# Optimization experiments

Hardware: AMD Instinct MI355X
Metric: run time of the kernel (lower is better)

Reference implementation:

```python
import jax, jax.numpy as jnp
import numpy as np

D_MODEL = 1024
NUM_HEAD = 16
D_HEAD = D_MODEL // NUM_HEAD


def setup_inputs() -> dict:
    key = jax.random.key(0)
    kx, kq, kk, kv, ko = jax.random.split(key, 5)
    x = jax.random.normal(kx, (2, 2048, D_MODEL), dtype=jnp.float32)
    p_q = jax.random.normal(kq, (D_MODEL, D_MODEL), dtype=jnp.float32)
    p_k = jax.random.normal(kk, (D_MODEL, D_MODEL), dtype=jnp.float32)
    p_v = jax.random.normal(kv, (D_MODEL, D_MODEL), dtype=jnp.float32)
    p_o = jax.random.normal(ko, (D_MODEL, D_MODEL), dtype=jnp.float32)
    return {"x": x, "p_q": p_q, "p_k": p_k, "p_v": p_v, "p_o": p_o}


def reference(x, p_q, p_k, p_v, p_o):
    B, S, _ = x.shape
    # project: weight viewed as [H, d_head, d_model]; out[b,h,s,d] = sum_m x[b,s,m] W[h,d,m]
    wq = p_q.reshape(NUM_HEAD, D_HEAD, D_MODEL)
    wk = p_k.reshape(NUM_HEAD, D_HEAD, D_MODEL)
    wv = p_v.reshape(NUM_HEAD, D_HEAD, D_MODEL)
    q = jnp.einsum('bsm,hdm->bhsd', x, wq)
    k = jnp.einsum('bsm,hdm->bhsd', x, wk)
    v = jnp.einsum('bsm,hdm->bhsd', x, wv)
    # full causal attention, scores scaled by 1/sqrt(d_head)
    scores = jnp.einsum('bhqd,bhkd->bhqk', q, k) / jnp.sqrt(jnp.float32(D_HEAD))
    causal = jnp.tril(jnp.ones((S, S), dtype=bool))
    scores = jnp.where(causal, scores, -jnp.inf)
    attn = jax.nn.softmax(scores, axis=-1)
    out = jnp.einsum('bhqk,bhkd->bhqd', attn, v)
    out = out.transpose(0, 2, 1, 3).reshape(B, S, D_MODEL)  # [B,S,H*d_head]
    # output proj: einsum '... d1, d2 d1 -> ... d2' == out @ p_o.T
    return jnp.einsum('bsm,nm->bsn', out, p_o)
```

## Files before the change

### kernel.cpp

```cpp
#include <hip/hip_runtime.h>
#include <stdint.h>

#define D_MODEL 1024
#define SEQ     2048
#define NHEAD   16
#define BATCH   2
#define NROWS   (BATCH*SEQ)

typedef _Float16 f16;
typedef _Float16 f16x8 __attribute__((ext_vector_type(8)));
typedef _Float16 f16x4 __attribute__((ext_vector_type(4)));
typedef __fp16   h16x2 __attribute__((ext_vector_type(2)));
typedef float    f32x4 __attribute__((ext_vector_type(4)));

#define MFMA16 __builtin_amdgcn_mfma_f32_16x16x32_f16

__device__ __forceinline__ void gload16(const void* g, void* l) {
  __builtin_amdgcn_global_load_lds(
      (const __attribute__((address_space(1))) void*)g,
      (__attribute__((address_space(3))) void*)l, 16, 0, 0);
}

__device__ __forceinline__ int pkh2(float a, float b) {
  union { h16x2 h; int i; } u;
  u.h = __builtin_amdgcn_cvt_pkrtz(a, b);
  return u.i;
}

__global__ void split4_kernel(const float* __restrict__ in, f16* __restrict__ hi,
                              f16* __restrict__ lo, int n4, float scale) {
  int i = blockIdx.x * blockDim.x + threadIdx.x;
  if (i >= n4) return;
  float4 v = reinterpret_cast<const float4*>(in)[i];
  v.x *= scale; v.y *= scale; v.z *= scale; v.w *= scale;
  f16x4 h, l4;
  h[0] = (f16)v.x; h[1] = (f16)v.y; h[2] = (f16)v.z; h[3] = (f16)v.w;
  l4[0] = (f16)(v.x - (float)h[0]);
  l4[1] = (f16)(v.y - (float)h[1]);
  l4[2] = (f16)(v.z - (float)h[2]);
  l4[3] = (f16)(v.w - (float)h[3]);
  *reinterpret_cast<f16x4*>(hi + 4*(size_t)i) = h;
  *reinterpret_cast<f16x4*>(lo + 4*(size_t)i) = l4;
}

__global__ void prep_w_kernel(const float* __restrict__ pq, const float* __restrict__ pk,
                              const float* __restrict__ pv, const float* __restrict__ po,
                              f16* __restrict__ wq_hi, f16* __restrict__ wq_lo,
                              f16* __restrict__ wk_hi, f16* __restrict__ wk_lo,
                              f16* __restrict__ wv_h,  f16* __restrict__ wo_h,
                              int n4, float qscale) {
  int i = blockIdx.x * blockDim.x + threadIdx.x;
  if (i >= n4) return;
  {
    float4 v = reinterpret_cast<const float4*>(pq)[i];
    v.x *= qscale; v.y *= qscale; v.z *= qscale; v.w *= qscale;
    f16x4 h, l4;
    h[0] = (f16)v.x; h[1] = (f16)v.y; h[2] = (f16)v.z; h[3] = (f16)v.w;
    l4[0] = (f16)(v.x - (float)h[0]); l4[1] = (f16)(v.y - (float)h[1]);
    l4[2] = (f16)(v.z - (float)h[2]); l4[3] = (f16)(v.w - (float)h[3]);
    *reinterpret_cast<f16x4*>(wq_hi + 4*(size_t)i) = h;
    *reinterpret_cast<f16x4*>(wq_lo + 4*(size_t)i) = l4;
  }
  {
    float4 v = reinterpret_cast<const float4*>(pk)[i];
    f16x4 h, l4;
    h[0] = (f16)v.x; h[1] = (f16)v.y; h[2] = (f16)v.z; h[3] = (f16)v.w;
    l4[0] = (f16)(v.x - (float)h[0]); l4[1] = (f16)(v.y - (float)h[1]);
    l4[2] = (f16)(v.z - (float)h[2]); l4[3] = (f16)(v.w - (float)h[3]);
    *reinterpret_cast<f16x4*>(wk_hi + 4*(size_t)i) = h;
    *reinterpret_cast<f16x4*>(wk_lo + 4*(size_t)i) = l4;
  }
  {
    float4 v = reinterpret_cast<const float4*>(pv)[i];
    f16x4 h;
    h[0] = (f16)v.x; h[1] = (f16)v.y; h[2] = (f16)v.z; h[3] = (f16)v.w;
    *reinterpret_cast<f16x4*>(wv_h + 4*(size_t)i) = h;
  }
  {
    float4 v = reinterpret_cast<const float4*>(po)[i];
    f16x4 h;
    h[0] = (f16)v.x; h[1] = (f16)v.y; h[2] = (f16)v.z; h[3] = (f16)v.w;
    *reinterpret_cast<f16x4*>(wo_h + 4*(size_t)i) = h;
  }
}

template<bool SPLIT_IN, bool SPLIT_OUT, bool F32_OUT, bool COLCHUNK>
__global__ __launch_bounds__(256, 2)
void gemm_nt(const f16* __restrict__ Ahi, const f16* __restrict__ Alo,
             const f16* __restrict__ Bhi, const f16* __restrict__ Blo,
             f16* __restrict__ Chi, f16* __restrict__ Clo, float* __restrict__ Cf,
             int M, int N, int K)
{
  constexpr int ALO_OFF = 8192;
  constexpr int B_OFF   = SPLIT_IN ? 16384 : 8192;
  constexpr int BLO_OFF = 20480;
  constexpr int STRIDE  = SPLIT_IN ? 24576 : 12288;
  __shared__ __align__(16) char smem[2 * STRIDE];

  const int tid = threadIdx.x;
  const int w = tid >> 6, l = tid & 63;
  const int wr = (w >> 1) * 64;
  const int wc = (w & 1) * 32;

  const int gx = gridDim.x, gy = gridDim.y;
  const int nwg = gx * gy;
  const int flat = blockIdx.y * gx + blockIdx.x;
  const int swz = (flat & 7) * (nwg >> 3) + (flat >> 3);
  const int bxn = COLCHUNK ? (swz / gy) : (swz % gx);
  const int byn = COLCHUNK ? (swz % gy) : (swz / gx);
  const int bm = byn * 128, bn = bxn * 64;

  f32x4 acc[4][2] = {};

  const int srow = tid >> 2;
  const int schunk = 8 * (((tid & 3) ^ ((srow >> 1) & 3)));

  auto stage = [&](int kt) {
    char* dst = smem + (kt & 1) * STRIDE;
    const int k0 = kt * 32;
    const f16* ga = Ahi + (size_t)(bm + srow) * K + k0 + schunk;
    gload16(ga,        dst + (w << 10));
    gload16(ga + 64*K, dst + 4096 + (w << 10));
    const f16* gb = Bhi + (size_t)(bn + srow) * K + k0 + schunk;
    gload16(gb,        dst + B_OFF + (w << 10));
    if (SPLIT_IN) {
      const f16* gal = Alo + (size_t)(bm + srow) * K + k0 + schunk;
      gload16(gal,        dst + ALO_OFF + (w << 10));
      gload16(gal + 64*K, dst + ALO_OFF + 4096 + (w << 10));
      const f16* gbl = Blo + (size_t)(bn + srow) * K + k0 + schunk;
      gload16(gbl,        dst + BLO_OFF + (w << 10));
    }
  };

  const int nkt = K >> 5;
  stage(0);

  for (int kt = 0; kt < nkt; kt++) {
    if (kt + 1 < nkt) {
      stage(kt + 1);
      if constexpr (SPLIT_IN) asm volatile("s_waitcnt vmcnt(6)" ::: "memory");
      else                    asm volatile("s_waitcnt vmcnt(3)" ::: "memory");
    } else {
      asm volatile("s_waitcnt vmcnt(0)" ::: "memory");
    }
    __builtin_amdgcn_s_barrier();

    const char* buf = smem + (kt & 1) * STRIDE;
    const int ar = (l & 15);
    const int ak = 16 * ((l >> 4) ^ ((ar >> 1) & 3));
    f16x8 a_hi[4], a_lo[4];
#pragma unroll
    for (int mi = 0; mi < 4; mi++) {
      a_hi[mi] = *(const f16x8*)(buf + (size_t)(wr + mi*16 + ar) * 64 + ak);
      if (SPLIT_IN)
        a_lo[mi] = *(const f16x8*)(buf + ALO_OFF + (size_t)(wr + mi*16 + ar) * 64 + ak);
    }
    __builtin_amdgcn_s_setprio(1);
#pragma unroll
    for (int ni = 0; ni < 2; ni++) {
      f16x8 b_hi = *(const f16x8*)(buf + B_OFF + (size_t)(wc + ni*16 + ar) * 64 + ak);
      f16x8 b_lo = {};
      if (SPLIT_IN)
        b_lo = *(const f16x8*)(buf + BLO_OFF + (size_t)(wc + ni*16 + ar) * 64 + ak);
#pragma unroll
      for (int mi = 0; mi < 4; mi++) {
        acc[mi][ni] = MFMA16(a_hi[mi], b_hi, acc[mi][ni], 0, 0, 0);
        if (SPLIT_IN) {
          acc[mi][ni] = MFMA16(a_hi[mi], b_lo, acc[mi][ni], 0, 0, 0);
          acc[mi][ni] = MFMA16(a_lo[mi], b_hi, acc[mi][ni], 0, 0, 0);
        }
      }
    }
    __builtin_amdgcn_s_setprio(0);
    __builtin_amdgcn_s_barrier();
  }

  const int crow0 = bm + wr + (l >> 4) * 4;
  const int ccol0 = bn + wc + (l & 15);
#pragma unroll
  for (int mi = 0; mi < 4; mi++) {
#pragma unroll
    for (int ni = 0; ni < 2; ni++) {
#pragma unroll
      for (int j = 0; j < 4; j++) {
        size_t idx = (size_t)(crow0 + mi*16 + j) * N + (ccol0 + ni*16);
        float v = acc[mi][ni][j];
        if (F32_OUT) {
          Cf[idx] = v;
        } else {
          f16 h = (f16)v;
          Chi[idx] = h;
          if (SPLIT_OUT) Clo[idx] = (f16)(v - (float)h);
        }
      }
    }
  }
}

__global__ __launch_bounds__(512, 4)
void attn_kernel(const f16* __restrict__ Qhi, const f16* __restrict__ Qlo,
                 const f16* __restrict__ Khi, const f16* __restrict__ Klo,
                 const f16* __restrict__ VT, f16* __restrict__ Out)
{
  __shared__ __align__(16) char smem[49152];

  const int tid = threadIdx.x, w = tid >> 6, l = tid & 63;
  const int g = l >> 4, q4 = l & 15;
  const int flat = blockIdx.x;
  const int xcd = flat & 7, slot = flat >> 3;
  const int r4 = slot >> 4;
  const int ii = slot & 15;
  const int bh = xcd * 4 + r4;
  const int qx = ((slot >> 5) & 1) ? (15 - ii) : ii;
  const int b = bh >> 4, h = bh & 15;
  const int q0 = qx * 128;
  const int qw = q0 + w * 16;
  const int bS = b * SEQ;
  const size_t hoff = (size_t)h * 64;
  const int niter = 2 * qx + 2;

  f16x8 qh[2], ql[2];
#pragma unroll
  for (int ks = 0; ks < 2; ks++) {
    const size_t base = (size_t)(bS + qw + q4) * D_MODEL + hoff + ks * 32 + g * 8;
    qh[ks] = *(const f16x8*)(Qhi + base);
    ql[ks] = *(const f16x8*)(Qlo + base);
  }

  f32x4 o[4] = {};
  float m_run = -INFINITY, l_run = 0.f;

  const int src_off = 8 * ((l & 7) ^ (l >> 3));
  const int rowloc = w * 8 + (l >> 3);

  auto stage = [&](int t) {
    char* dst = smem + (t & 1) * 24576;
    const int kv0 = t * 64;
    const size_t krow = (size_t)(bS + kv0 + rowloc) * D_MODEL + hoff + src_off;
    gload16(Khi + krow, dst + (w << 10));
    gload16(Klo + krow, dst + 8192 + (w << 10));
    const size_t vrow = (hoff + rowloc) * (size_t)NROWS + bS + kv0 + src_off;
    gload16(VT + vrow, dst + 16384 + (w << 10));
  };

  const int idx_lo = (q4 + 32 * (g & 1)) * 4;
  const int idx_hi = idx_lo + 64;
  const bool upper = (l >= 32);

  stage(0);

  for (int t = 0; t < niter; t++) {
    if (t + 1 < niter) {
      stage(t + 1);
      asm volatile("s_waitcnt vmcnt(3)" ::: "memory");
    } else {
      asm volatile("s_waitcnt vmcnt(0)" ::: "memory");
    }
    __builtin_amdgcn_s_barrier();

    const int kv0 = t * 64;
    if (kv0 <= qw + 15) {
      const char* buf = smem + (t & 1) * 24576;

      f32x4 s[4] = {};
      __builtin_amdgcn_s_setprio(1);
#pragma unroll
      for (int ni = 0; ni < 4; ni++) {
        const int row = ni * 16 + q4;
#pragma unroll
        for (int ks = 0; ks < 2; ks++) {
          const int boff = row * 128 + 16 * ((ks * 4 + g) ^ (row & 7));
          f16x8 kh8 = *(const f16x8*)(buf + boff);
          f16x8 kl8 = *(const f16x8*)(buf + 8192 + boff);
          s[ni] = MFMA16(kh8, qh[ks], s[ni], 0, 0, 0);
          s[ni] = MFMA16(kh8, ql[ks], s[ni], 0, 0, 0);
          s[ni] = MFMA16(kl8, qh[ks], s[ni], 0, 0, 0);
        }
      }
      __builtin_amdgcn_s_setprio(0);

      const bool need_mask = (kv0 + 63) > qw;
      const int q_abs = qw + q4;
      float p[4][4];
      float pm = -INFINITY;
#pragma unroll
      for (int ni = 0; ni < 4; ni++)
#pragma unroll
        for (int j = 0; j < 4; j++) {
          float v = s[ni][j];
          if (need_mask && (kv0 + ni*16 + 4*g + j) > q_abs) v = -INFINITY;
          p[ni][j] = v;
          pm = fmaxf(pm, v);
        }
      pm = fmaxf(pm, __shfl_xor(pm, 16));
      pm = fmaxf(pm, __shfl_xor(pm, 32));

      const float mn = fmaxf(m_run, pm);
      const float sc = __builtin_amdgcn_exp2f(m_run - mn);
      m_run = mn;
      float ps = 0.f;
#pragma unroll
      for (int ni = 0; ni < 4; ni++)
#pragma unroll
        for (int j = 0; j < 4; j++) {
          const float e = __builtin_amdgcn_exp2f(p[ni][j] - mn);
          p[ni][j] = e;
          ps += e;
        }
      ps += __shfl_xor(ps, 16);
      ps += __shfl_xor(ps, 32);
      l_run = l_run * sc + ps;
#pragma unroll
      for (int nd = 0; nd < 4; nd++)
#pragma unroll
        for (int j = 0; j < 4; j++) o[nd][j] *= sc;

      f16x8 pa[2];
#pragma unroll
      for (int h2 = 0; h2 < 2; h2++) {
        const int pk0 = pkh2(p[2*h2][0],   p[2*h2][1]);
        const int pk1 = pkh2(p[2*h2][2],   p[2*h2][3]);
        const int pk2 = pkh2(p[2*h2+1][0], p[2*h2+1][1]);
        const int pk3 = pkh2(p[2*h2+1][2], p[2*h2+1][3]);
        const int b0l = __builtin_amdgcn_ds_bpermute(idx_lo, pk0);
        const int b2l = __builtin_amdgcn_ds_bpermute(idx_lo, pk2);
        const int b1l = __builtin_amdgcn_ds_bpermute(idx_lo, pk1);
        const int b3l = __builtin_amdgcn_ds_bpermute(idx_lo, pk3);
        const int b0h = __builtin_amdgcn_ds_bpermute(idx_hi, pk0);
        const int b2h = __builtin_amdgcn_ds_bpermute(idx_hi, pk2);
        const int b1h = __builtin_amdgcn_ds_bpermute(idx_hi, pk1);
        const int b3h = __builtin_amdgcn_ds_bpermute(idx_hi, pk3);
        union { int u[4]; f16x8 v; } pu;
        pu.u[0] = upper ? b2l : b0l;
        pu.u[1] = upper ? b3l : b1l;
        pu.u[2] = upper ? b2h : b0h;
        pu.u[3] = upper ? b3h : b1h;
        pa[h2] = pu.v;
      }

      __builtin_amdgcn_s_setprio(1);
#pragma unroll
      for (int nd = 0; nd < 4; nd++) {
        const int d = nd * 16 + q4;
#pragma unroll
        for (int h2 = 0; h2 < 2; h2++) {
          f16x8 bv = *(const f16x8*)(buf + 16384 + d * 128 + 16 * ((h2 * 4 + g) ^ (d & 7)));
          o[nd] = MFMA16(bv, pa[h2], o[nd], 0, 0, 0);
        }
      }
      __builtin_amdgcn_s_setprio(0);
    }
    __builtin_amdgcn_s_barrier();
  }

  const float inv = 1.0f / l_run;
  const size_t rowb = (size_t)(bS + qw + q4) * D_MODEL + hoff;
#pragma unroll
  for (int nd = 0; nd < 4; nd++) {
    f16x4 v;
#pragma unroll
    for (int j = 0; j < 4; j++) v[j] = (f16)(o[nd][j] * inv);
    *reinterpret_cast<f16x4*>(Out + rowb + nd * 16 + 4 * g) = v;
  }
}

extern "C" void kernel_launch(void* const* d_in, const int* in_sizes, int n_in,
                              void* d_out, int out_size, void* d_ws, size_t ws_size,
                              hipStream_t stream) {
  const float* x  = (const float*)d_in[0];
  const float* pq = (const float*)d_in[1];
  const float* pk = (const float*)d_in[2];
  const float* pv = (const float*)d_in[3];
  const float* po = (const float*)d_in[4];
  float* out = (float*)d_out;

  char* ws = (char*)d_ws;
  size_t off = 0;
  auto alloc = [&](size_t elems) {
    f16* p = (f16*)(ws + off);
    off += ((elems * 2 + 255) & ~(size_t)255);
    return p;
  };
  f16* x_hi  = alloc((size_t)NROWS * D_MODEL);
  f16* x_lo  = alloc((size_t)NROWS * D_MODEL);
  f16* wq_hi = alloc((size_t)D_MODEL * D_MODEL);
  f16* wq_lo = alloc((size_t)D_MODEL * D_MODEL);
  f16* wk_hi = alloc((size_t)D_MODEL * D_MODEL);
  f16* wk_lo = alloc((size_t)D_MODEL * D_MODEL);
  f16* wv_h  = alloc((size_t)D_MODEL * D_MODEL);
  f16* wo_h  = alloc((size_t)D_MODEL * D_MODEL);
  f16* q_hi  = alloc((size_t)NROWS * D_MODEL);
  f16* q_lo  = alloc((size_t)NROWS * D_MODEL);
  f16* k_hi  = alloc((size_t)NROWS * D_MODEL);
  f16* k_lo  = alloc((size_t)NROWS * D_MODEL);
  f16* vt    = alloc((size_t)NROWS * D_MODEL);
  f16* ao    = alloc((size_t)NROWS * D_MODEL);

  const int n4x = NROWS * D_MODEL / 4;
  const int n4w = D_MODEL * D_MODEL / 4;
  const float qscale = 0.125f * 1.44269504088896f;
  split4_kernel<<<n4x/256, 256, 0, stream>>>(x, x_hi, x_lo, n4x, 1.0f);
  prep_w_kernel<<<n4w/256, 256, 0, stream>>>(pq, pk, pv, po,
                                             wq_hi, wq_lo, wk_hi, wk_lo, wv_h, wo_h,
                                             n4w, qscale);

  dim3 gg(D_MODEL/64, NROWS/128);
  gemm_nt<true,  true,  false, false><<<gg, 256, 0, stream>>>(x_hi, x_lo, wq_hi, wq_lo, q_hi, q_lo, nullptr, NROWS, D_MODEL, D_MODEL);
  gemm_nt<true,  true,  false, false><<<gg, 256, 0, stream>>>(x_hi, x_lo, wk_hi, wk_lo, k_hi, k_lo, nullptr, NROWS, D_MODEL, D_MODEL);
  dim3 gv(NROWS/64, D_MODEL/128);
  gemm_nt<false, false, false, true><<<gv, 256, 0, stream>>>(wv_h, nullptr, x_hi, nullptr, vt, nullptr, nullptr, D_MODEL, NROWS, D_MODEL);

  attn_kernel<<<dim3(512), 512, 0, stream>>>(q_hi, q_lo, k_hi, k_lo, vt, ao);

  gemm_nt<false, false, true, false><<<gg, 256, 0, stream>>>(ao, nullptr, wo_h, nullptr, nullptr, nullptr, out, NROWS, D_MODEL, D_MODEL);
}
```

Measured before the change: 178.5 us.

## Software-pipeline QK^T one tile ahead and skip rescale when max grows little

Restructures the attention loop so K tiles are double-buffered and V tiles triple-buffered, with loads issued two tiles ahead and the QK^T MFMAs for tile t+1 computed before the softmax/PV of tile t. It also adds a lazy rescale: the running max and output rescale are updated only when some lane's new max exceeds the old one by more than 8 (in log2 units). The aim is to overlap memory latency and MFMA work with softmax and to cut per-iteration rescale ALU work. In exchange it uses more LDS (56KB), which may lower occupancy, adds an extra barrier per iteration, and lets probabilities exceed 1 by up to 2^8 before being converted to fp16.

```diff
diff --git a/kernel.cpp b/kernel.cpp
--- a/kernel.cpp
+++ b/kernel.cpp
@@ -202,7 +202,7 @@
                  const f16* __restrict__ Khi, const f16* __restrict__ Klo,
                  const f16* __restrict__ VT, f16* __restrict__ Out)
 {
-  __shared__ __align__(16) char smem[49152];
+  __shared__ __align__(16) char smem[57344];
 
   const int tid = threadIdx.x, w = tid >> 6, l = tid & 63;
   const int g = l >> 4, q4 = l & 15;
@@ -234,13 +234,36 @@
   const int rowloc = w * 8 + (l >> 3);
 
   auto stage = [&](int t) {
-    char* dst = smem + (t & 1) * 24576;
     const int kv0 = t * 64;
+    char* kdst = smem + (t & 1) * 16384 + (w << 10);
     const size_t krow = (size_t)(bS + kv0 + rowloc) * D_MODEL + hoff + src_off;
-    gload16(Khi + krow, dst + (w << 10));
-    gload16(Klo + krow, dst + 8192 + (w << 10));
+    gload16(Khi + krow, kdst);
+    gload16(Klo + krow, kdst + 8192);
+    char* vdst = smem + 32768 + (t % 3) * 8192 + (w << 10);
     const size_t vrow = (hoff + rowloc) * (size_t)NROWS + bS + kv0 + src_off;
-    gload16(VT + vrow, dst + 16384 + (w << 10));
+    gload16(VT + vrow, vdst);
+  };
+
+  f32x4 scur[4] = {};
+  auto qkt = [&](int t) {
+    const char* kb = smem + (t & 1) * 16384;
+    __builtin_amdgcn_s_setprio(1);
+#pragma unroll
+    for (int ni = 0; ni < 4; ni++) {
+      const int row = ni * 16 + q4;
+      f32x4 acc = {};
+#pragma unroll
+      for (int ks = 0; ks < 2; ks++) {
+        const int boff = row * 128 + 16 * ((ks * 4 + g) ^ (row & 7));
+        f16x8 kh8 = *(const f16x8*)(kb + boff);
+        f16x8 kl8 = *(const f16x8*)(kb + 8192 + boff);
+        acc = MFMA16(kh8, qh[ks], acc, 0, 0, 0);
+        acc = MFMA16(kh8, ql[ks], acc, 0, 0, 0);
+        acc = MFMA16(kl8, qh[ks], acc, 0, 0, 0);
+      }
+      scur[ni] = acc;
+    }
+    __builtin_amdgcn_s_setprio(0);
   };
 
   const int idx_lo = (q4 + 32 * (g & 1)) * 4;
@@ -248,37 +271,19 @@
   const bool upper = (l >= 32);
 
   stage(0);
+  stage(1);
+  asm volatile("s_waitcnt vmcnt(3)" ::: "memory");
+  __builtin_amdgcn_s_barrier();
+  qkt(0);
+  __builtin_amdgcn_s_barrier();
 
   for (int t = 0; t < niter; t++) {
-    if (t + 1 < niter) {
-      stage(t + 1);
-      asm volatile("s_waitcnt vmcnt(3)" ::: "memory");
-    } else {
-      asm volatile("s_waitcnt vmcnt(0)" ::: "memory");
-    }
-    __builtin_amdgcn_s_barrier();
+    const bool hasn = (t + 1 < niter);
+    const bool st2  = (t + 2 < niter);
+    if (st2) stage(t + 2);
 
     const int kv0 = t * 64;
     if (kv0 <= qw + 15) {
-      const char* buf = smem + (t & 1) * 24576;
-
-      f32x4 s[4] = {};
-      __builtin_amdgcn_s_setprio(1);
-#pragma unroll
-      for (int ni = 0; ni < 4; ni++) {
-        const int row = ni * 16 + q4;
-#pragma unroll
-        for (int ks = 0; ks < 2; ks++) {
-          const int boff = row * 128 + 16 * ((ks * 4 + g) ^ (row & 7));
-          f16x8 kh8 = *(const f16x8*)(buf + boff);
-          f16x8 kl8 = *(const f16x8*)(buf + 8192 + boff);
-          s[ni] = MFMA16(kh8, qh[ks], s[ni], 0, 0, 0);
-          s[ni] = MFMA16(kh8, ql[ks], s[ni], 0, 0, 0);
-          s[ni] = MFMA16(kl8, qh[ks], s[ni], 0, 0, 0);
-        }
-      }
-      __builtin_amdgcn_s_setprio(0);
-
       const bool need_mask = (kv0 + 63) > qw;
       const int q_abs = qw + q4;
       float p[4][4];
@@ -287,7 +292,7 @@
       for (int ni = 0; ni < 4; ni++)
 #pragma unroll
         for (int j = 0; j < 4; j++) {
-          float v = s[ni][j];
+          float v = scur[ni][j];
           if (need_mask && (kv0 + ni*16 + 4*g + j) > q_abs) v = -INFINITY;
           p[ni][j] = v;
           pm = fmaxf(pm, v);
@@ -295,25 +300,28 @@
       pm = fmaxf(pm, __shfl_xor(pm, 16));
       pm = fmaxf(pm, __shfl_xor(pm, 32));
 
-      const float mn = fmaxf(m_run, pm);
-      const float sc = __builtin_amdgcn_exp2f(m_run - mn);
-      m_run = mn;
+      if (!__all(pm - m_run <= 8.0f)) {
+        const float mn = fmaxf(m_run, pm);
+        const float sc = __builtin_amdgcn_exp2f(m_run - mn);
+        m_run = mn;
+        l_run *= sc;
+#pragma unroll
+        for (int nd = 0; nd < 4; nd++)
+#pragma unroll
+          for (int j = 0; j < 4; j++) o[nd][j] *= sc;
+      }
       float ps = 0.f;
 #pragma unroll
       for (int ni = 0; ni < 4; ni++)
 #pragma unroll
         for (int j = 0; j < 4; j++) {
-          const float e = __builtin_amdgcn_exp2f(p[ni][j] - mn);
+          const float e = __builtin_amdgcn_exp2f(p[ni][j] - m_run);
           p[ni][j] = e;
           ps += e;
         }
       ps += __shfl_xor(ps, 16);
       ps += __shfl_xor(ps, 32);
-      l_run = l_run * sc + ps;
-#pragma unroll
-      for (int nd = 0; nd < 4; nd++)
-#pragma unroll
-        for (int j = 0; j < 4; j++) o[nd][j] *= sc;
+      l_run += ps;
 
       f16x8 pa[2];
 #pragma unroll
@@ -338,19 +346,27 @@
         pa[h2] = pu.v;
       }
 
+      const char* vb = smem + 32768 + (t % 3) * 8192;
       __builtin_amdgcn_s_setprio(1);
 #pragma unroll
       for (int nd = 0; nd < 4; nd++) {
         const int d = nd * 16 + q4;
 #pragma unroll
         for (int h2 = 0; h2 < 2; h2++) {
-          f16x8 bv = *(const f16x8*)(buf + 16384 + d * 128 + 16 * ((h2 * 4 + g) ^ (d & 7)));
+          f16x8 bv = *(const f16x8*)(vb + d * 128 + 16 * ((h2 * 4 + g) ^ (d & 7)));
           o[nd] = MFMA16(bv, pa[h2], o[nd], 0, 0, 0);
         }
       }
       __builtin_amdgcn_s_setprio(0);
     }
-    __builtin_amdgcn_s_barrier();
+
+    if (hasn) {
+      if (st2) asm volatile("s_waitcnt vmcnt(3)" ::: "memory");
+      else     asm volatile("s_waitcnt vmcnt(0)" ::: "memory");
+      __builtin_amdgcn_s_barrier();
+      if (64 * (t + 1) <= qw + 15) qkt(t + 1);
+      __builtin_amdgcn_s_barrier();
+    }
   }
 
   const float inv = 1.0f / l_run;
```

Result: slower. 186.4 us (+4.4%).

## Pair causal query tiles per block with split-KV wave groups and lazy rescale

Applied to the files above, without the earlier changes.

Each block now handles two 64-row query tiles, one near the start and its mirror near the end, so every block does the same amount of causal work. The block's 8 waves form two groups that first process their own tiles, then split the shared tail of KV tiles between them, and finally merge their partial softmax states through shared memory. KV tiles shrink to 32 keys with a 4-deep LDS ring staged by a subset of waves. The online-softmax rescale is skipped while the running max grows by no more than 8. This targets load imbalance and pipeline depth, at the cost of more barriers, smaller MFMA batches per iteration and a merge step.

```diff
diff --git a/kernel.cpp b/kernel.cpp
--- a/kernel.cpp
+++ b/kernel.cpp
@@ -206,161 +206,224 @@
 
   const int tid = threadIdx.x, w = tid >> 6, l = tid & 63;
   const int g = l >> 4, q4 = l & 15;
+  const int wi = w & 3, grp = w >> 2;
   const int flat = blockIdx.x;
   const int xcd = flat & 7, slot = flat >> 3;
-  const int r4 = slot >> 4;
-  const int ii = slot & 15;
-  const int bh = xcd * 4 + r4;
-  const int qx = ((slot >> 5) & 1) ? (15 - ii) : ii;
+  const int bh = xcd * 4 + (slot >> 4);
+  const int c = slot & 15;
   const int b = bh >> 4, h = bh & 15;
-  const int q0 = qx * 128;
-  const int qw = q0 + w * 16;
   const int bS = b * SEQ;
   const size_t hoff = (size_t)h * 64;
-  const int niter = 2 * qx + 2;
+  const int T  = 64 - 2 * c;
+  const int P1 = 2 * c + 2;
+  const int P2 = 31 - 2 * c;
+
+  int qw = (grp ? (31 - c) : c) * 64 + wi * 16;
 
   f16x8 qh[2], ql[2];
-#pragma unroll
-  for (int ks = 0; ks < 2; ks++) {
-    const size_t base = (size_t)(bS + qw + q4) * D_MODEL + hoff + ks * 32 + g * 8;
-    qh[ks] = *(const f16x8*)(Qhi + base);
-    ql[ks] = *(const f16x8*)(Qlo + base);
-  }
+  auto loadQ = [&]() {
+#pragma unroll
+    for (int ks = 0; ks < 2; ks++) {
+      const size_t base = (size_t)(bS + qw + q4) * D_MODEL + hoff + ks * 32 + g * 8;
+      qh[ks] = *(const f16x8*)(Qhi + base);
+      ql[ks] = *(const f16x8*)(Qlo + base);
+    }
+  };
+  loadQ();
 
   f32x4 o[4] = {};
   float m_run = -INFINITY, l_run = 0.f;
 
-  const int src_off = 8 * ((l & 7) ^ (l >> 3));
-  const int rowloc = w * 8 + (l >> 3);
+  const int k_src = 8 * ((l & 7) ^ (l >> 3));
+  const int v_src = 8 * ((l & 3) ^ ((l >> 2) & 3));
 
   auto stage = [&](int t) {
-    char* dst = smem + (t & 1) * 24576;
-    const int kv0 = t * 64;
-    const size_t krow = (size_t)(bS + kv0 + rowloc) * D_MODEL + hoff + src_off;
-    gload16(Khi + krow, dst + (w << 10));
-    gload16(Klo + krow, dst + 8192 + (w << 10));
-    const size_t vrow = (hoff + rowloc) * (size_t)NROWS + bS + kv0 + src_off;
-    gload16(VT + vrow, dst + 16384 + (w << 10));
+    const int kv0 = t * 32;
+    char* sb = smem + (t & 3) * 12288;
+    if (w < 4) {
+      const f16* src = (w < 2) ? Khi : Klo;
+      char* dstc = sb + ((w < 2) ? 0 : 4096);
+      const int wi2 = w & 1;
+#pragma unroll
+      for (int gi = 0; gi < 2; gi++) {
+        const int sub = 2 * wi2 + gi;
+        const int row = 8 * sub + (l >> 3);
+        gload16(src + (size_t)(bS + kv0 + row) * D_MODEL + hoff + k_src,
+                dstc + sub * 1024);
+      }
+    } else if (w < 6) {
+      const int wi2 = w - 4;
+#pragma unroll
+      for (int gi = 0; gi < 2; gi++) {
+        const int sub = 2 * wi2 + gi;
+        const int drow = 16 * sub + (l >> 2);
+        gload16(VT + (hoff + drow) * (size_t)NROWS + bS + kv0 + v_src,
+                sb + 8192 + sub * 1024);
+      }
+    }
   };
 
   const int idx_lo = (q4 + 32 * (g & 1)) * 4;
   const int idx_hi = idx_lo + 64;
   const bool upper = (l >= 32);
 
-  stage(0);
-
-  for (int t = 0; t < niter; t++) {
-    if (t + 1 < niter) {
-      stage(t + 1);
-      asm volatile("s_waitcnt vmcnt(3)" ::: "memory");
-    } else {
-      asm volatile("s_waitcnt vmcnt(0)" ::: "memory");
-    }
-    __builtin_amdgcn_s_barrier();
-
-    const int kv0 = t * 64;
-    if (kv0 <= qw + 15) {
-      const char* buf = smem + (t & 1) * 24576;
-
-      f32x4 s[4] = {};
-      __builtin_amdgcn_s_setprio(1);
-#pragma unroll
-      for (int ni = 0; ni < 4; ni++) {
-        const int row = ni * 16 + q4;
-#pragma unroll
-        for (int ks = 0; ks < 2; ks++) {
-          const int boff = row * 128 + 16 * ((ks * 4 + g) ^ (row & 7));
-          f16x8 kh8 = *(const f16x8*)(buf + boff);
-          f16x8 kl8 = *(const f16x8*)(buf + 8192 + boff);
-          s[ni] = MFMA16(kh8, qh[ks], s[ni], 0, 0, 0);
-          s[ni] = MFMA16(kh8, ql[ks], s[ni], 0, 0, 0);
-          s[ni] = MFMA16(kl8, qh[ks], s[ni], 0, 0, 0);
-        }
-      }
-      __builtin_amdgcn_s_setprio(0);
-
-      const bool need_mask = (kv0 + 63) > qw;
-      const int q_abs = qw + q4;
-      float p[4][4];
-      float pm = -INFINITY;
-#pragma unroll
-      for (int ni = 0; ni < 4; ni++)
-#pragma unroll
-        for (int j = 0; j < 4; j++) {
-          float v = s[ni][j];
-          if (need_mask && (kv0 + ni*16 + 4*g + j) > q_abs) v = -INFINITY;
-          p[ni][j] = v;
-          pm = fmaxf(pm, v);
-        }
-      pm = fmaxf(pm, __shfl_xor(pm, 16));
-      pm = fmaxf(pm, __shfl_xor(pm, 32));
-
+  auto compute = [&](int t) {
+    const char* sb = smem + (t & 3) * 12288;
+    const int kv0 = t * 32;
+
+    f32x4 s[2] = {};
+    __builtin_amdgcn_s_setprio(1);
+#pragma unroll
+    for (int ni = 0; ni < 2; ni++) {
+      const int row = ni * 16 + q4;
+#pragma unroll
+      for (int ks = 0; ks < 2; ks++) {
+        const int boff = row * 128 + 16 * ((ks * 4 + g) ^ (row & 7));
+        f16x8 kh8 = *(const f16x8*)(sb + boff);
+        f16x8 kl8 = *(const f16x8*)(sb + 4096 + boff);
+        s[ni] = MFMA16(kh8, qh[ks], s[ni], 0, 0, 0);
+        s[ni] = MFMA16(kh8, ql[ks], s[ni], 0, 0, 0);
+        s[ni] = MFMA16(kl8, qh[ks], s[ni], 0, 0, 0);
+      }
+    }
+    __builtin_amdgcn_s_setprio(0);
+
+    const bool need_mask = (kv0 + 31) > qw;
+    const int q_abs = qw + q4;
+    float p[2][4];
+    float pm = -INFINITY;
+#pragma unroll
+    for (int ni = 0; ni < 2; ni++)
+#pragma unroll
+      for (int j = 0; j < 4; j++) {
+        float v = s[ni][j];
+        if (need_mask && (kv0 + ni * 16 + 4 * g + j) > q_abs) v = -INFINITY;
+        p[ni][j] = v;
+        pm = fmaxf(pm, v);
+      }
+    pm = fmaxf(pm, __shfl_xor(pm, 16));
+    pm = fmaxf(pm, __shfl_xor(pm, 32));
+
+    if (!__all(pm - m_run <= 8.0f)) {
       const float mn = fmaxf(m_run, pm);
       const float sc = __builtin_amdgcn_exp2f(m_run - mn);
       m_run = mn;
-      float ps = 0.f;
-#pragma unroll
-      for (int ni = 0; ni < 4; ni++)
-#pragma unroll
-        for (int j = 0; j < 4; j++) {
-          const float e = __builtin_amdgcn_exp2f(p[ni][j] - mn);
-          p[ni][j] = e;
-          ps += e;
-        }
-      ps += __shfl_xor(ps, 16);
-      ps += __shfl_xor(ps, 32);
-      l_run = l_run * sc + ps;
+      l_run *= sc;
 #pragma unroll
       for (int nd = 0; nd < 4; nd++)
 #pragma unroll
         for (int j = 0; j < 4; j++) o[nd][j] *= sc;
-
-      f16x8 pa[2];
-#pragma unroll
-      for (int h2 = 0; h2 < 2; h2++) {
-        const int pk0 = pkh2(p[2*h2][0],   p[2*h2][1]);
-        const int pk1 = pkh2(p[2*h2][2],   p[2*h2][3]);
-        const int pk2 = pkh2(p[2*h2+1][0], p[2*h2+1][1]);
-        const int pk3 = pkh2(p[2*h2+1][2], p[2*h2+1][3]);
-        const int b0l = __builtin_amdgcn_ds_bpermute(idx_lo, pk0);
-        const int b2l = __builtin_amdgcn_ds_bpermute(idx_lo, pk2);
-        const int b1l = __builtin_amdgcn_ds_bpermute(idx_lo, pk1);
-        const int b3l = __builtin_amdgcn_ds_bpermute(idx_lo, pk3);
-        const int b0h = __builtin_amdgcn_ds_bpermute(idx_hi, pk0);
-        const int b2h = __builtin_amdgcn_ds_bpermute(idx_hi, pk2);
-        const int b1h = __builtin_amdgcn_ds_bpermute(idx_hi, pk1);
-        const int b3h = __builtin_amdgcn_ds_bpermute(idx_hi, pk3);
-        union { int u[4]; f16x8 v; } pu;
-        pu.u[0] = upper ? b2l : b0l;
-        pu.u[1] = upper ? b3l : b1l;
-        pu.u[2] = upper ? b2h : b0h;
-        pu.u[3] = upper ? b3h : b1h;
-        pa[h2] = pu.v;
-      }
-
-      __builtin_amdgcn_s_setprio(1);
-#pragma unroll
-      for (int nd = 0; nd < 4; nd++) {
-        const int d = nd * 16 + q4;
-#pragma unroll
-        for (int h2 = 0; h2 < 2; h2++) {
-          f16x8 bv = *(const f16x8*)(buf + 16384 + d * 128 + 16 * ((h2 * 4 + g) ^ (d & 7)));
-          o[nd] = MFMA16(bv, pa[h2], o[nd], 0, 0, 0);
-        }
-      }
-      __builtin_amdgcn_s_setprio(0);
-    }
-    __builtin_amdgcn_s_barrier();
-  }
-
-  const float inv = 1.0f / l_run;
-  const size_t rowb = (size_t)(bS + qw + q4) * D_MODEL + hoff;
-#pragma unroll
-  for (int nd = 0; nd < 4; nd++) {
-    f16x4 v;
-#pragma unroll
-    for (int j = 0; j < 4; j++) v[j] = (f16)(o[nd][j] * inv);
-    *reinterpret_cast<f16x4*>(Out + rowb + nd * 16 + 4 * g) = v;
+    }
+    float ps = 0.f;
+#pragma unroll
+    for (int ni = 0; ni < 2; ni++)
+#pragma unroll
+      for (int j = 0; j < 4; j++) {
+        const float e = __builtin_amdgcn_exp2f(p[ni][j] - m_run);
+        p[ni][j] = e;
+        ps += e;
+      }
+    ps += __shfl_xor(ps, 16);
+    ps += __shfl_xor(ps, 32);
+    l_run += ps;
+
+    const int pk0 = pkh2(p[0][0], p[0][1]);
+    const int pk1 = pkh2(p[0][2], p[0][3]);
+    const int pk2 = pkh2(p[1][0], p[1][1]);
+    const int pk3 = pkh2(p[1][2], p[1][3]);
+    const int b0l = __builtin_amdgcn_ds_bpermute(idx_lo, pk0);
+    const int b2l = __builtin_amdgcn_ds_bpermute(idx_lo, pk2);
+    const int b1l = __builtin_amdgcn_ds_bpermute(idx_lo, pk1);
+    const int b3l = __builtin_amdgcn_ds_bpermute(idx_lo, pk3);
+    const int b0h = __builtin_amdgcn_ds_bpermute(idx_hi, pk0);
+    const int b2h = __builtin_amdgcn_ds_bpermute(idx_hi, pk2);
+    const int b1h = __builtin_amdgcn_ds_bpermute(idx_hi, pk1);
+    const int b3h = __builtin_amdgcn_ds_bpermute(idx_hi, pk3);
+    union { int u[4]; f16x8 v; } pu;
+    pu.u[0] = upper ? b2l : b0l;
+    pu.u[1] = upper ? b3l : b1l;
+    pu.u[2] = upper ? b2h : b0h;
+    pu.u[3] = upper ? b3h : b1h;
+    const f16x8 pa = pu.v;
+
+    __builtin_amdgcn_s_setprio(1);
+#pragma unroll
+    for (int nd = 0; nd < 4; nd++) {
+      const int d = nd * 16 + q4;
+      f16x8 bv = *(const f16x8*)(sb + 8192 + d * 64 + 16 * (g ^ (d & 3)));
+      o[nd] = MFMA16(bv, pa, o[nd], 0, 0, 0);
+    }
+    __builtin_amdgcn_s_setprio(0);
+  };
+
+  stage(0);
+  stage(1);
+
+  for (int t = 0; t < P1; t++) {
+    stage(t + 2);
+    asm volatile("s_waitcnt vmcnt(4)" ::: "memory");
+    __builtin_amdgcn_s_barrier();
+    compute(t);
+    __builtin_amdgcn_s_barrier();
+  }
+
+  if (grp == 0) {
+    const float inv = 1.0f / l_run;
+    const size_t rowb = (size_t)(bS + qw + q4) * D_MODEL + hoff;
+#pragma unroll
+    for (int nd = 0; nd < 4; nd++) {
+      f16x4 v;
+#pragma unroll
+      for (int j = 0; j < 4; j++) v[j] = (f16)(o[nd][j] * inv);
+      *reinterpret_cast<f16x4*>(Out + rowb + nd * 16 + 4 * g) = v;
+    }
+    qw = (31 - c) * 64 + wi * 16;
+    loadQ();
+#pragma unroll
+    for (int nd = 0; nd < 4; nd++)
+#pragma unroll
+      for (int j = 0; j < 4; j++) o[nd][j] = 0.f;
+    m_run = -INFINITY;
+    l_run = 0.f;
+  }
+
+  for (int j = 0; j < P2; j++) {
+    const int u = P1 + 2 * j;
+    const bool st = (u + 3) < T;
+    if (st) { stage(u + 2); stage(u + 3); }
+    if (st) asm volatile("s_waitcnt vmcnt(4)" ::: "memory");
+    else    asm volatile("s_waitcnt vmcnt(0)" ::: "memory");
+    __builtin_amdgcn_s_barrier();
+    compute(u + grp);
+    __builtin_amdgcn_s_barrier();
+  }
+
+  if (grp == 0) {
+    float* mb = (float*)smem + wi * 1152 + l * 18;
+#pragma unroll
+    for (int nd = 0; nd < 4; nd++)
+#pragma unroll
+      for (int j = 0; j < 4; j++) mb[nd * 4 + j] = o[nd][j];
+    mb[16] = m_run;
+    mb[17] = l_run;
+  }
+  __syncthreads();
+  if (grp == 1) {
+    const float* mb = (const float*)smem + wi * 1152 + l * 18;
+    const float m2 = mb[16], l2 = mb[17];
+    const float mm = fmaxf(m_run, m2);
+    const float a1 = __builtin_amdgcn_exp2f(m_run - mm);
+    const float a2 = __builtin_amdgcn_exp2f(m2 - mm);
+    const float inv = 1.0f / (l_run * a1 + l2 * a2);
+    const size_t rowb = (size_t)(bS + qw + q4) * D_MODEL + hoff;
+#pragma unroll
+    for (int nd = 0; nd < 4; nd++) {
+      f16x4 v;
+#pragma unroll
+      for (int j = 0; j < 4; j++)
+        v[j] = (f16)((o[nd][j] * a1 + mb[nd * 4 + j] * a2) * inv);
+      *reinterpret_cast<f16x4*>(Out + rowb + nd * 16 + 4 * g) = v;
+    }
   }
 }
 
```

After: 180.3 us. No clear change (+1.0%).
